# Optimization experiments

Hardware: AMD Instinct MI355X
Metric: run time of the kernel (lower is better)

The kernel has to match this reference:

```python
import jax, jax.numpy as jnp
import numpy as np
from jax import lax

B, T, C, F = 64, 1152, 64, 8
L_DP, N_DP = 24, 12
NUM_CLASSES = 4


def setup_inputs() -> dict:
    key = jax.random.key(0)
    ks = jax.random.split(key, 8)
    num_chunks = T // L_DP
    return {
        "L_norm": jax.random.normal(ks[0], (B, C, C), jnp.float32) / C,
        "X_seq": jax.random.normal(ks[1], (B, T, C, F), jnp.float32),
        "deterministic": 1,
        "conv_kernel": jax.random.normal(ks[2], (32, 1, F, 8), jnp.float32) * 0.06,  # HWIO
        "ln_scale": jnp.ones((8,), jnp.float32),
        "ln_bias": jnp.zeros((8,), jnp.float32),
        "spatial_w": jax.random.normal(ks[3], (64, 4), jnp.float32) * 0.17,
        "W1": jax.random.normal(ks[4], (num_chunks * 64, 32), jnp.float32) * 0.02,
        "b1": jnp.zeros((32,), jnp.float32),
        "W2": jax.random.normal(ks[5], (32, NUM_CLASSES), jnp.float32) * 0.1,
        "b2": jnp.zeros((NUM_CLASSES,), jnp.float32),
    }


def _spike(x):
    return jnp.where(x > 0, 1.0, 0.0).astype(x.dtype)


def reference(L_norm, X_seq, deterministic, conv_kernel, ln_scale, ln_bias,
              spatial_w, W1, b1, W2, b2):
    # temporal conv over (T, C) spatial dims, F -> 8 channels, SAME padding
    ann = lax.conv_general_dilated(
        X_seq, conv_kernel, window_strides=(1, 1), padding="SAME",
        dimension_numbers=("NHWC", "HWIO", "NHWC"))
    # LayerNorm over last (feature) axis, eps=1e-6 (flax default)
    mu = jnp.mean(ann, axis=-1, keepdims=True)
    var = jnp.mean(jnp.square(ann - mu), axis=-1, keepdims=True)
    ann = (ann - mu) * lax.rsqrt(var + 1e-6) * ln_scale + ln_bias
    ann = jax.nn.relu(ann)
    # graph propagation + channel-spatial projection
    gx = jnp.einsum("bnm,btmf->btnf", L_norm, ann)          # (B,T,64,8)
    gx_csp = jnp.einsum("btcf,cs->btsf", gx, spatial_w)     # (B,T,4,8)
    snn_in = gx_csp.reshape(B, T, 32)

    # two-layer LIF recurrence over time (strictly sequential)
    def step(carry, x_t):
        mem1, mem2, mem_out = carry
        mem1 = mem1 * 0.8 + x_t
        spk1 = _spike(mem1 - 0.5)
        mem1 = mem1 - spk1 * 0.5
        mem2 = mem2 * 0.9 + spk1
        spk2 = _spike(mem2 - 0.5)
        mem2 = mem2 - spk2 * 0.5
        mem_out = mem_out * 0.95 + spk2
        return (mem1, mem2, mem_out), (mem_out, spk1, spk2)

    mem0 = jnp.zeros((B, 32), snn_in.dtype)
    _, (pot, spk1, spk2) = lax.scan(step, (mem0, mem0, mem0),
                                    jnp.swapaxes(snn_in, 0, 1))
    pot = jnp.swapaxes(pot, 0, 1)                           # (B,T,32)

    chunks = pot.reshape(B, T // L_DP, L_DP, 32)
    start_mean = jnp.mean(chunks[:, :, :N_DP, :], axis=2)
    end_mean = jnp.mean(chunks[:, :, -N_DP:, :], axis=2)
    flat = jnp.concatenate([start_mean, end_mean], axis=-1).reshape(B, -1)

    y = jax.nn.gelu(flat @ W1 + b1)   # flax nn.gelu default approximate=True
    logits = y @ W2 + b2
    firing_rate = (jnp.mean(spk1) + jnp.mean(spk2)) / 2.0
    return logits, firing_rate
```

## Files before the change

kernel.cpp:

```cpp
#include <hip/hip_runtime.h>
#include <hip/hip_fp16.h>
#include <math.h>

#define T_SEQ 1152

typedef _Float16 f16x8 __attribute__((ext_vector_type(8)));
typedef float f32x4 __attribute__((ext_vector_type(4)));

__global__ void mKernel(const float* __restrict__ L, const float* __restrict__ sw,
                        float* __restrict__ Mbuf) {
  int b = blockIdx.x, tid = threadIdx.x;
  int s = tid >> 6, m = tid & 63;
  float a = 0.f;
  #pragma unroll 4
  for (int n = 0; n < 64; ++n)
    a = fmaf(sw[n * 4 + s], L[(b * 64 + n) * 64 + m], a);
  Mbuf[b * 256 + m * 4 + s] = a;
}

__global__ __launch_bounds__(256, 4)
void convKernel(const float* __restrict__ X, const float* __restrict__ Kw,
                const float* __restrict__ lnS, const float* __restrict__ lnB,
                const float* __restrict__ Mbuf, float* __restrict__ snn) {
  __shared__ int4   XS[8 * 97];
  __shared__ float4 hT4[512];

  const int bid  = blockIdx.x;
  const int b    = bid / 18;
  const int tile = bid - b * 18;
  const int t0   = tile * 64;
  const int tid  = threadIdx.x;
  const int lane = tid & 63;
  const int wid  = tid >> 6;
  const int h    = wid & 1;
  const int g    = wid >> 1;
  const int w32  = h * 32;
  const int tcol = lane & 15;
  const int rg   = lane >> 4;
  const int fq   = rg & 1;
  const int tloc = tcol + ((rg >> 1) << 4);

  const int rA = lane & 15;
  const int fr = rA & 7;
  const int sh16 = (rA >> 3) << 4;
  f16x8 ka[12];
  #pragma unroll
  for (int q = 0; q < 12; ++q) {
    const int khs = 4 * q + rg - sh16;
    #pragma unroll
    for (int j = 0; j < 8; ++j) {
      float kv = (khs >= 0 && khs < 32) ? Kw[khs * 64 + j * 8 + fr] : 0.f;
      ka[q][j] = (_Float16)kv;
    }
  }

  const int tpt   = lane >> 1;
  const int cslot = lane & 1;

  const int sc2 = tid & 7;
  int stl[3]; long gb[3]; bool tv[3];
  #pragma unroll
  for (int k = 0; k < 3; ++k) {
    stl[k] = (tid >> 3) + 32 * k;
    int tt = t0 - 15 + stl[k];
    tv[k] = (stl[k] < 95) && (tt >= 0) && (tt < T_SEQ);
    gb[k] = (long)tt * 512 + sc2 * 8;
  }
  const float* xb = X + (size_t)(b * T_SEQ) * 512;

  float pacc[4][8];
  #pragma unroll
  for (int s = 0; s < 4; ++s)
    #pragma unroll
    for (int f = 0; f < 8; ++f) pacc[s][f] = 0.f;

  #pragma unroll 1
  for (int part = 0; part < 8; ++part) {
    #pragma unroll
    for (int k = 0; k < 3; ++k) {
      if (stl[k] < 95) {
        float4 a0 = make_float4(0.f, 0.f, 0.f, 0.f), a1 = a0;
        if (tv[k]) {
          const float* p = xb + gb[k] + part * 64;
          a0 = *(const float4*)p;
          a1 = *(const float4*)(p + 4);
        }
        unsigned u0 = __builtin_bit_cast(unsigned, __float22half2_rn(make_float2(a0.x, a0.y)));
        unsigned u1 = __builtin_bit_cast(unsigned, __float22half2_rn(make_float2(a0.z, a0.w)));
        unsigned u2 = __builtin_bit_cast(unsigned, __float22half2_rn(make_float2(a1.x, a1.y)));
        unsigned u3 = __builtin_bit_cast(unsigned, __float22half2_rn(make_float2(a1.z, a1.w)));
        int4 v; v.x = (int)u0; v.y = (int)u1; v.z = (int)u2; v.w = (int)u3;
        XS[sc2 * 97 + stl[k]] = v;
      }
    }
    __syncthreads();

    #pragma unroll 1
    for (int pair = 0; pair < 2; ++pair) {
      #pragma unroll
      for (int cp = 0; cp < 2; ++cp) {
        const int cc = pair * 2 + cp;
        f32x4 acc = {0.f, 0.f, 0.f, 0.f};
        const int rb = (g * 4 + cc) * 97 + w32 + tcol + rg;
        #pragma unroll
        for (int q = 0; q < 12; ++q) {
          f16x8 xf = __builtin_bit_cast(f16x8, XS[rb + 4 * q]);
          acc = __builtin_amdgcn_mfma_f32_16x16x32_f16(ka[q], xf, acc, 0, 0, 0);
        }
        float4 st; st.x = acc[0]; st.y = acc[1]; st.z = acc[2]; st.w = acc[3];
        hT4[wid * 128 + cp * 64 + fq * 32 + tloc] = st;
      }

      {
        const int c2l = pair * 2 + cslot;
        float4 lo = hT4[wid * 128 + cslot * 64 + tpt];
        float4 hi = hT4[wid * 128 + cslot * 64 + 32 + tpt];
        float hv[8] = { lo.x, lo.y, lo.z, lo.w, hi.x, hi.y, hi.z, hi.w };
        float mu = 0.f;
        #pragma unroll
        for (int f = 0; f < 8; ++f) mu += hv[f];
        mu *= 0.125f;
        float var = 0.f;
        #pragma unroll
        for (int f = 0; f < 8; ++f) { float d = hv[f] - mu; hv[f] = d; var = fmaf(d, d, var); }
        float rs = 1.0f / sqrtf(var * 0.125f + 1e-6f);
        const int c = part * 8 + g * 4 + c2l;
        const float4 Mc = *(const float4*)(Mbuf + b * 256 + c * 4);
        #pragma unroll
        for (int f = 0; f < 8; ++f) {
          float hh = fmaxf(fmaf(hv[f] * rs, lnS[f], lnB[f]), 0.f);
          pacc[0][f] = fmaf(hh, Mc.x, pacc[0][f]);
          pacc[1][f] = fmaf(hh, Mc.y, pacc[1][f]);
          pacc[2][f] = fmaf(hh, Mc.z, pacc[2][f]);
          pacc[3][f] = fmaf(hh, Mc.w, pacc[3][f]);
        }
      }
    }
    __syncthreads();
  }

  #pragma unroll
  for (int s = 0; s < 4; ++s)
    #pragma unroll
    for (int f = 0; f < 8; ++f)
      pacc[s][f] += __shfl_xor(pacc[s][f], 1, 64);

  float* RedF = (float*)&XS[0];
  const int trow = h * 32 + tpt;
  if (g == 0 && cslot == 0) {
    #pragma unroll
    for (int s = 0; s < 4; ++s)
      #pragma unroll
      for (int f = 0; f < 8; ++f)
        RedF[trow * 33 + s * 8 + f] = pacc[s][f];
  }
  __syncthreads();
  if (g == 1 && cslot == 0) {
    float* op = snn + ((size_t)b * T_SEQ + t0 + trow) * 32;
    #pragma unroll
    for (int s = 0; s < 4; ++s) {
      float4 v0, v1;
      v0.x = pacc[s][0] + RedF[trow * 33 + s * 8 + 0];
      v0.y = pacc[s][1] + RedF[trow * 33 + s * 8 + 1];
      v0.z = pacc[s][2] + RedF[trow * 33 + s * 8 + 2];
      v0.w = pacc[s][3] + RedF[trow * 33 + s * 8 + 3];
      v1.x = pacc[s][4] + RedF[trow * 33 + s * 8 + 4];
      v1.y = pacc[s][5] + RedF[trow * 33 + s * 8 + 5];
      v1.z = pacc[s][6] + RedF[trow * 33 + s * 8 + 6];
      v1.w = pacc[s][7] + RedF[trow * 33 + s * 8 + 7];
      *(float4*)(op + s * 8)     = v0;
      *(float4*)(op + s * 8 + 4) = v1;
    }
  }
}

__global__ __launch_bounds__(64, 1)
void scanKernel(const float* __restrict__ snn, float* __restrict__ flat,
                float* __restrict__ spkPart) {
  const int tid = threadIdx.x;
  const int j = tid & 31;
  const int b = blockIdx.x * 2 + (tid >> 5);
  const float* base = snn + (size_t)b * T_SEQ * 32 + j;

  float m1 = 0.f, m2 = 0.f, mo = 0.f, s1 = 0.f, s2 = 0.f;
  float cur[24], nxt[24];
  #pragma unroll
  for (int u = 0; u < 24; ++u) cur[u] = base[(size_t)u * 32];

  #pragma unroll 1
  for (int ch = 0; ch < 48; ++ch) {
    if (ch < 47) {
      #pragma unroll
      for (int u = 0; u < 24; ++u) nxt[u] = base[(size_t)((ch + 1) * 24 + u) * 32];
    }
    float aS = 0.f, aE = 0.f;
    #pragma unroll
    for (int u = 0; u < 24; ++u) {
      m1 = m1 * 0.8f + cur[u];
      float sp1 = (m1 > 0.5f) ? 1.f : 0.f;  m1 -= sp1 * 0.5f;
      m2 = m2 * 0.9f + sp1;
      float sp2 = (m2 > 0.5f) ? 1.f : 0.f;  m2 -= sp2 * 0.5f;
      mo = mo * 0.95f + sp2;
      s1 += sp1; s2 += sp2;
      if (u < 12) aS += mo; else aE += mo;
    }
    flat[b * 3072 + ch * 64 + j]      = aS / 12.0f;
    flat[b * 3072 + ch * 64 + 32 + j] = aE / 12.0f;
    if (ch < 47) {
      #pragma unroll
      for (int u = 0; u < 24; ++u) cur[u] = nxt[u];
    }
  }
  for (int off = 16; off > 0; off >>= 1) {
    s1 += __shfl_down(s1, off, 32);
    s2 += __shfl_down(s2, off, 32);
  }
  if (j == 0) { spkPart[b * 2] = s1; spkPart[b * 2 + 1] = s2; }
}

__global__ void mlpKernel(const float* __restrict__ flat, const float* __restrict__ W1,
                          const float* __restrict__ b1, const float* __restrict__ W2,
                          const float* __restrict__ b2, const float* __restrict__ spkPart,
                          float* __restrict__ out) {
  if (blockIdx.x == 64) {
    if (threadIdx.x == 0) {
      float s1 = 0.f, s2 = 0.f;
      for (int i = 0; i < 64; ++i) { s1 += spkPart[2*i]; s2 += spkPart[2*i+1]; }
      out[256] = (s1 + s2) * 0.5f / (64.0f * 1152.0f * 32.0f);
    }
    return;
  }
  const int b = blockIdx.x;
  const int tid = threadIdx.x;
  const int u = tid & 31, kc = tid >> 5;
  __shared__ float red[256];
  __shared__ float ys[32];
  float p = 0.f;
  const int kbeg = kc * 384, kend = kbeg + 384;
  #pragma unroll 4
  for (int k = kbeg; k < kend; ++k)
    p = fmaf(flat[b*3072 + k], W1[k*32 + u], p);
  red[tid] = p;
  __syncthreads();
  if (kc == 0) {
    float y = b1[u];
    #pragma unroll
    for (int q = 0; q < 8; ++q) y += red[q*32 + u];
    float y3 = y * y * y;
    float th = tanhf(0.7978845608028654f * (y + 0.044715f * y3));
    ys[u] = 0.5f * y * (1.0f + th);
  }
  __syncthreads();
  if (tid < 4) {
    float accv = b2[tid];
    #pragma unroll
    for (int q = 0; q < 32; ++q) accv = fmaf(ys[q], W2[q*4 + tid], accv);
    out[b*4 + tid] = accv;
  }
}

extern "C" void kernel_launch(void* const* d_in, const int* in_sizes, int n_in,
                              void* d_out, int out_size, void* d_ws, size_t ws_size,
                              hipStream_t stream) {
  const float* L   = (const float*)d_in[0];
  const float* X   = (const float*)d_in[1];
  const float* Kw  = (const float*)d_in[3];
  const float* lnS = (const float*)d_in[4];
  const float* lnB = (const float*)d_in[5];
  const float* sw  = (const float*)d_in[6];
  const float* W1  = (const float*)d_in[7];
  const float* b1  = (const float*)d_in[8];
  const float* W2  = (const float*)d_in[9];
  const float* b2  = (const float*)d_in[10];

  float* ws   = (float*)d_ws;
  float* Mbuf = ws;
  float* snn  = Mbuf + 16384;
  float* flat = snn + 2359296;
  float* spk  = flat + 196608;
  float* out  = (float*)d_out;

  mKernel<<<64, 256, 0, stream>>>(L, sw, Mbuf);
  convKernel<<<1152, 256, 0, stream>>>(X, Kw, lnS, lnB, Mbuf, snn);
  scanKernel<<<32, 64, 0, stream>>>(snn, flat, spk);
  mlpKernel<<<65, 256, 0, stream>>>(flat, W1, b1, W2, b2, spk, out);
}
```

Before: 153.4 us.

## Halve conv time tile to 32 steps and split channels across all four waves

The conv kernel's time tile shrinks from 64 to 32 steps, doubling the grid to 2304 blocks. Each wave now covers all 32 time steps for two channels per part instead of half the time range for four channels, and the final cross-wave reduction sums four wave partials through LDS in two passes. The aim is more blocks for occupancy and load balance, at the cost of a larger relative halo (63 staged rows for 32 outputs vs 95 for 64), which means more redundant global reads of X.

```diff
diff --git a/kernel.cpp b/kernel.cpp
--- a/kernel.cpp
+++ b/kernel.cpp
@@ -22,19 +22,16 @@
 void convKernel(const float* __restrict__ X, const float* __restrict__ Kw,
                 const float* __restrict__ lnS, const float* __restrict__ lnB,
                 const float* __restrict__ Mbuf, float* __restrict__ snn) {
-  __shared__ int4   XS[8 * 97];
+  __shared__ int4   XS[8 * 65];
   __shared__ float4 hT4[512];
 
   const int bid  = blockIdx.x;
-  const int b    = bid / 18;
-  const int tile = bid - b * 18;
-  const int t0   = tile * 64;
+  const int b    = bid / 36;
+  const int tile = bid - b * 36;
+  const int t0   = tile * 32;
   const int tid  = threadIdx.x;
   const int lane = tid & 63;
   const int wid  = tid >> 6;
-  const int h    = wid & 1;
-  const int g    = wid >> 1;
-  const int w32  = h * 32;
   const int tcol = lane & 15;
   const int rg   = lane >> 4;
   const int fq   = rg & 1;
@@ -58,14 +55,12 @@
   const int cslot = lane & 1;
 
   const int sc2 = tid & 7;
-  int stl[3]; long gb[3]; bool tv[3];
-  #pragma unroll
-  for (int k = 0; k < 3; ++k) {
-    stl[k] = (tid >> 3) + 32 * k;
-    int tt = t0 - 15 + stl[k];
-    tv[k] = (stl[k] < 95) && (tt >= 0) && (tt < T_SEQ);
-    gb[k] = (long)tt * 512 + sc2 * 8;
-  }
+  const int srow0 = tid >> 3;
+  const int srow1 = srow0 + 32;
+  const int st0 = t0 - 15 + srow0;
+  const int st1 = t0 - 15 + srow1;
+  const bool v0 = (st0 >= 0) && (st0 < T_SEQ);
+  const bool v1 = (srow1 < 63) && (st1 >= 0) && (st1 < T_SEQ);
   const float* xb = X + (size_t)(b * T_SEQ) * 512;
 
   float pacc[4][8];
@@ -76,64 +71,65 @@
 
   #pragma unroll 1
   for (int part = 0; part < 8; ++part) {
-    #pragma unroll
-    for (int k = 0; k < 3; ++k) {
-      if (stl[k] < 95) {
-        float4 a0 = make_float4(0.f, 0.f, 0.f, 0.f), a1 = a0;
-        if (tv[k]) {
-          const float* p = xb + gb[k] + part * 64;
-          a0 = *(const float4*)p;
-          a1 = *(const float4*)(p + 4);
-        }
+    {
+      const float* xp = xb + (part * 8 + sc2) * 8;
+      float4 a0 = make_float4(0.f, 0.f, 0.f, 0.f), a1 = a0;
+      float4 b0 = a0, b1 = a0;
+      if (v0) { const float* p = xp + (size_t)st0 * 512; a0 = *(const float4*)p; a1 = *(const float4*)(p + 4); }
+      if (v1) { const float* p = xp + (size_t)st1 * 512; b0 = *(const float4*)p; b1 = *(const float4*)(p + 4); }
+      {
         unsigned u0 = __builtin_bit_cast(unsigned, __float22half2_rn(make_float2(a0.x, a0.y)));
         unsigned u1 = __builtin_bit_cast(unsigned, __float22half2_rn(make_float2(a0.z, a0.w)));
         unsigned u2 = __builtin_bit_cast(unsigned, __float22half2_rn(make_float2(a1.x, a1.y)));
         unsigned u3 = __builtin_bit_cast(unsigned, __float22half2_rn(make_float2(a1.z, a1.w)));
         int4 v; v.x = (int)u0; v.y = (int)u1; v.z = (int)u2; v.w = (int)u3;
-        XS[sc2 * 97 + stl[k]] = v;
-      }
-    }
-    __syncthreads();
-
-    #pragma unroll 1
-    for (int pair = 0; pair < 2; ++pair) {
-      #pragma unroll
-      for (int cp = 0; cp < 2; ++cp) {
-        const int cc = pair * 2 + cp;
-        f32x4 acc = {0.f, 0.f, 0.f, 0.f};
-        const int rb = (g * 4 + cc) * 97 + w32 + tcol + rg;
-        #pragma unroll
-        for (int q = 0; q < 12; ++q) {
-          f16x8 xf = __builtin_bit_cast(f16x8, XS[rb + 4 * q]);
-          acc = __builtin_amdgcn_mfma_f32_16x16x32_f16(ka[q], xf, acc, 0, 0, 0);
-        }
-        float4 st; st.x = acc[0]; st.y = acc[1]; st.z = acc[2]; st.w = acc[3];
-        hT4[wid * 128 + cp * 64 + fq * 32 + tloc] = st;
-      }
-
-      {
-        const int c2l = pair * 2 + cslot;
-        float4 lo = hT4[wid * 128 + cslot * 64 + tpt];
-        float4 hi = hT4[wid * 128 + cslot * 64 + 32 + tpt];
-        float hv[8] = { lo.x, lo.y, lo.z, lo.w, hi.x, hi.y, hi.z, hi.w };
-        float mu = 0.f;
-        #pragma unroll
-        for (int f = 0; f < 8; ++f) mu += hv[f];
-        mu *= 0.125f;
-        float var = 0.f;
-        #pragma unroll
-        for (int f = 0; f < 8; ++f) { float d = hv[f] - mu; hv[f] = d; var = fmaf(d, d, var); }
-        float rs = 1.0f / sqrtf(var * 0.125f + 1e-6f);
-        const int c = part * 8 + g * 4 + c2l;
-        const float4 Mc = *(const float4*)(Mbuf + b * 256 + c * 4);
-        #pragma unroll
-        for (int f = 0; f < 8; ++f) {
-          float hh = fmaxf(fmaf(hv[f] * rs, lnS[f], lnB[f]), 0.f);
-          pacc[0][f] = fmaf(hh, Mc.x, pacc[0][f]);
-          pacc[1][f] = fmaf(hh, Mc.y, pacc[1][f]);
-          pacc[2][f] = fmaf(hh, Mc.z, pacc[2][f]);
-          pacc[3][f] = fmaf(hh, Mc.w, pacc[3][f]);
-        }
+        XS[sc2 * 65 + srow0] = v;
+      }
+      if (srow1 < 63) {
+        unsigned u0 = __builtin_bit_cast(unsigned, __float22half2_rn(make_float2(b0.x, b0.y)));
+        unsigned u1 = __builtin_bit_cast(unsigned, __float22half2_rn(make_float2(b0.z, b0.w)));
+        unsigned u2 = __builtin_bit_cast(unsigned, __float22half2_rn(make_float2(b1.x, b1.y)));
+        unsigned u3 = __builtin_bit_cast(unsigned, __float22half2_rn(make_float2(b1.z, b1.w)));
+        int4 v; v.x = (int)u0; v.y = (int)u1; v.z = (int)u2; v.w = (int)u3;
+        XS[sc2 * 65 + srow1] = v;
+      }
+    }
+    __syncthreads();
+
+    #pragma unroll
+    for (int cp = 0; cp < 2; ++cp) {
+      f32x4 acc = {0.f, 0.f, 0.f, 0.f};
+      const int rb = (wid * 2 + cp) * 65 + tcol + rg;
+      #pragma unroll
+      for (int q = 0; q < 12; ++q) {
+        f16x8 xf = __builtin_bit_cast(f16x8, XS[rb + 4 * q]);
+        acc = __builtin_amdgcn_mfma_f32_16x16x32_f16(ka[q], xf, acc, 0, 0, 0);
+      }
+      float4 st; st.x = acc[0]; st.y = acc[1]; st.z = acc[2]; st.w = acc[3];
+      hT4[wid * 128 + cp * 64 + fq * 32 + tloc] = st;
+    }
+
+    {
+      float4 lo = hT4[wid * 128 + cslot * 64 + tpt];
+      float4 hi = hT4[wid * 128 + cslot * 64 + 32 + tpt];
+      float hv[8] = { lo.x, lo.y, lo.z, lo.w, hi.x, hi.y, hi.z, hi.w };
+      float mu = 0.f;
+      #pragma unroll
+      for (int f = 0; f < 8; ++f) mu += hv[f];
+      mu *= 0.125f;
+      float var = 0.f;
+      #pragma unroll
+      for (int f = 0; f < 8; ++f) { float d = hv[f] - mu; hv[f] = d; var = fmaf(d, d, var); }
+      float rs = 1.0f / sqrtf(var * 0.125f + 1e-6f);
+      const int c = part * 8 + wid * 2 + cslot;
+      const float4 Mc = *(const float4*)(Mbuf + b * 256 + c * 4);
+      #pragma unroll
+      for (int f = 0; f < 8; ++f) {
+        float hh = fmaxf(fmaf(hv[f] * rs, lnS[f], lnB[f]), 0.f);
+        pacc[0][f] = fmaf(hh, Mc.x, pacc[0][f]);
+        pacc[1][f] = fmaf(hh, Mc.y, pacc[1][f]);
+        pacc[2][f] = fmaf(hh, Mc.z, pacc[2][f]);
+        pacc[3][f] = fmaf(hh, Mc.w, pacc[3][f]);
       }
     }
     __syncthreads();
@@ -145,31 +141,33 @@
     for (int f = 0; f < 8; ++f)
       pacc[s][f] += __shfl_xor(pacc[s][f], 1, 64);
 
-  float* RedF = (float*)&XS[0];
-  const int trow = h * 32 + tpt;
-  if (g == 0 && cslot == 0) {
-    #pragma unroll
-    for (int s = 0; s < 4; ++s)
-      #pragma unroll
-      for (int f = 0; f < 8; ++f)
-        RedF[trow * 33 + s * 8 + f] = pacc[s][f];
-  }
-  __syncthreads();
-  if (g == 1 && cslot == 0) {
-    float* op = snn + ((size_t)b * T_SEQ + t0 + trow) * 32;
-    #pragma unroll
-    for (int s = 0; s < 4; ++s) {
-      float4 v0, v1;
-      v0.x = pacc[s][0] + RedF[trow * 33 + s * 8 + 0];
-      v0.y = pacc[s][1] + RedF[trow * 33 + s * 8 + 1];
-      v0.z = pacc[s][2] + RedF[trow * 33 + s * 8 + 2];
-      v0.w = pacc[s][3] + RedF[trow * 33 + s * 8 + 3];
-      v1.x = pacc[s][4] + RedF[trow * 33 + s * 8 + 4];
-      v1.y = pacc[s][5] + RedF[trow * 33 + s * 8 + 5];
-      v1.z = pacc[s][6] + RedF[trow * 33 + s * 8 + 6];
-      v1.w = pacc[s][7] + RedF[trow * 33 + s * 8 + 7];
-      *(float4*)(op + s * 8)     = v0;
-      *(float4*)(op + s * 8 + 4) = v1;
+  float* R = (float*)hT4;
+  #pragma unroll 1
+  for (int pass = 0; pass < 2; ++pass) {
+    __syncthreads();
+    if (wid > 0 && cslot == 0) {
+      #pragma unroll
+      for (int s2 = 0; s2 < 2; ++s2)
+        #pragma unroll
+        for (int f = 0; f < 8; ++f)
+          R[((wid - 1) * 32 + tpt) * 16 + s2 * 8 + f] = pacc[pass * 2 + s2][f];
+    }
+    __syncthreads();
+    if (wid == 0 && cslot == 0) {
+      float* op = snn + ((size_t)b * T_SEQ + t0 + tpt) * 32;
+      #pragma unroll
+      for (int s2 = 0; s2 < 2; ++s2) {
+        const int s = pass * 2 + s2;
+        float v[8];
+        #pragma unroll
+        for (int f = 0; f < 8; ++f)
+          v[f] = pacc[s][f]
+               + R[(0 * 32 + tpt) * 16 + s2 * 8 + f]
+               + R[(1 * 32 + tpt) * 16 + s2 * 8 + f]
+               + R[(2 * 32 + tpt) * 16 + s2 * 8 + f];
+        *(float4*)(op + s * 8)     = make_float4(v[0], v[1], v[2], v[3]);
+        *(float4*)(op + s * 8 + 4) = make_float4(v[4], v[5], v[6], v[7]);
+      }
     }
   }
 }
@@ -281,7 +279,7 @@
   float* out  = (float*)d_out;
 
   mKernel<<<64, 256, 0, stream>>>(L, sw, Mbuf);
-  convKernel<<<1152, 256, 0, stream>>>(X, Kw, lnS, lnB, Mbuf, snn);
+  convKernel<<<2304, 256, 0, stream>>>(X, Kw, lnS, lnB, Mbuf, snn);
   scanKernel<<<32, 64, 0, stream>>>(snn, flat, spk);
   mlpKernel<<<65, 256, 0, stream>>>(flat, W1, b1, W2, b2, spk, out);
 }
```

After: 243.0 us. +58.4%, slower.
